# Kernel tuning notes

Measured on AMD Instinct MI355X. Metric: run time of the kernel, lower is better.

Reference implementation:

```python
import jax, jax.numpy as jnp
import numpy as np

D_IN = 1024
D_OUT = 1024
NUM_HEADS = 16
DIM_HEAD = D_OUT // NUM_HEADS


def setup_inputs() -> dict:
    key = jax.random.key(0)
    ks = jax.random.split(key, 6)
    s = 0.02
    x = jax.random.normal(ks[0], (2, 2048, D_IN), dtype=jnp.float32)
    Wk = jax.random.normal(ks[1], (D_IN, D_OUT), dtype=jnp.float32) * s
    Wq = jax.random.normal(ks[2], (D_IN, D_OUT), dtype=jnp.float32) * s
    Wv = jax.random.normal(ks[3], (D_IN, D_OUT), dtype=jnp.float32) * s
    Wo = jax.random.normal(ks[4], (D_OUT, D_OUT), dtype=jnp.float32) * s
    bo = jax.random.normal(ks[5], (D_OUT,), dtype=jnp.float32) * s
    return {"x": x, "Wk": Wk, "Wq": Wq, "Wv": Wv, "Wo": Wo, "bo": bo}


def reference(x, Wk, Wq, Wv, Wo, bo):
    B, S, _ = x.shape
    # projections -> [B, H, S, Dh]
    def split_heads(t):
        return t.reshape(B, S, NUM_HEADS, DIM_HEAD).transpose(0, 2, 1, 3)
    q = split_heads(x @ Wq)
    k = split_heads(x @ Wk)
    v = split_heads(x @ Wv)
    # NOTE: source uses non-in-place masked_fill whose result is discarded,
    # so NO causal mask is actually applied (faithful reproduction).
    scores = jnp.einsum("bhqd,bhkd->bhqk", q, k) / jnp.sqrt(jnp.float32(DIM_HEAD))
    wgts = jax.nn.softmax(scores, axis=-1)  # dropout = identity (eval mode)
    ctx = jnp.einsum("bhqk,bhkd->bhqd", wgts, v)
    ctx = ctx.transpose(0, 2, 1, 3).reshape(B, S, D_OUT)
    return ctx @ Wo + bo
```

## Files before the change

kernel.cpp:

```cpp
#include <hip/hip_runtime.h>
#include <stdint.h>

typedef short bf16x8 __attribute__((ext_vector_type(8)));
typedef float f32x4  __attribute__((ext_vector_type(4)));
typedef unsigned int u32x4 __attribute__((ext_vector_type(4)));
typedef unsigned int u32x2 __attribute__((ext_vector_type(2)));

__device__ __forceinline__ unsigned short f2bf(float f) {
  unsigned int u = __builtin_bit_cast(unsigned int, f) + 0x8000u;
  return (unsigned short)(u >> 16);
}
__device__ __forceinline__ unsigned int pack2bf(float a, float b) {
  unsigned int ua = __builtin_bit_cast(unsigned int, a) + 0x8000u;
  unsigned int ub = __builtin_bit_cast(unsigned int, b) + 0x8000u;
  return __builtin_amdgcn_perm(ub, ua, 0x07060302);
}

__device__ __forceinline__ void gl2lds16(const void* g, void* l) {
  __builtin_amdgcn_global_load_lds(
      (const __attribute__((address_space(1))) void*)g,
      (__attribute__((address_space(3))) void*)l, 16, 0, 0);
}

template <int N> __device__ __forceinline__ void wait_vmcnt() {
  asm volatile("s_waitcnt vmcnt(%0)" ::"n"(N) : "memory");
}

__global__ __launch_bounds__(256) void cast_x_k(const float* __restrict__ x,
                                                unsigned short* __restrict__ xb) {
  int i = blockIdx.x * 256 + threadIdx.x;
  float4 v = ((const float4*)x)[i];
  u32x2 o;
  o.x = pack2bf(v.x, v.y);
  o.y = pack2bf(v.z, v.w);
  ((u32x2*)xb)[i] = o;
}

__global__ __launch_bounds__(256) void castT_k(
    const float* __restrict__ Wq, const float* __restrict__ Wk,
    const float* __restrict__ Wv, const float* __restrict__ Wo,
    unsigned short* __restrict__ Tq, unsigned short* __restrict__ Tk,
    unsigned short* __restrict__ Tv, unsigned short* __restrict__ To) {
  __shared__ float tile[32][33];
  const int z = blockIdx.z;
  const float* W = (z == 0) ? Wq : (z == 1) ? Wk : (z == 2) ? Wv : Wo;
  unsigned short* T = (z == 0) ? Tq : (z == 1) ? Tk : (z == 2) ? Tv : To;
  const int tx = threadIdx.x, ty = threadIdx.y;
  const int n0 = blockIdx.x * 32, k0 = blockIdx.y * 32;
#pragma unroll
  for (int j = 0; j < 32; j += 8)
    tile[ty + j][tx] = W[(size_t)(k0 + ty + j) * 1024 + n0 + tx];
  __syncthreads();
#pragma unroll
  for (int j = 0; j < 32; j += 8)
    T[(size_t)(n0 + ty + j) * 1024 + k0 + tx] = f2bf(tile[tx][ty + j]);
}

template <int MODE, int TN>
__global__ __launch_bounds__(256, 2) void gemm_bt_k(const unsigned short* __restrict__ A,
                                                    const unsigned short* __restrict__ B,
                                                    void* __restrict__ C,
                                                    const float* __restrict__ bias,
                                                    int K) {
  __shared__ alignas(16) short lA[4][512 * 8];
  __shared__ alignas(16) short lB[4][128 * TN * 8];
  constexpr int PT = 2 + TN / 2;
  const int tid = threadIdx.x;
  const int wid = tid >> 6, lane = tid & 63;
  const int l15 = lane & 15, quad = lane >> 4;
  const int waveM = wid >> 1, waveN = wid & 1;
  const int bm = blockIdx.y * 128, bn = blockIdx.x * (32 * TN);

  f32x4 acc[4][TN];
#pragma unroll
  for (int i = 0; i < 4; ++i)
#pragma unroll
    for (int j = 0; j < TN; ++j) acc[i][j] = (f32x4){0.f, 0.f, 0.f, 0.f};

  auto stage = [&](int kk, short* la, short* lb) {
#pragma unroll
    for (int j = 0; j < 2; ++j) {
      int c = tid + 256 * j;
      int row = ((c >> 6) << 4) | (c & 15);
      int ch = (c >> 4) & 3;
      gl2lds16(A + (size_t)(bm + row) * K + kk + ch * 8, &la[(c & ~63) * 8]);
    }
#pragma unroll
    for (int j = 0; j < TN / 2; ++j) {
      int c = tid + 256 * j;
      int row = ((c >> 6) << 4) | (c & 15);
      int ch = (c >> 4) & 3;
      gl2lds16(B + (size_t)(bn + row) * K + kk + ch * 8, &lb[(c & ~63) * 8]);
    }
  };

  auto compute = [&](const short* la, const short* lb) {
    bf16x8 af[4], bfr[TN];
#pragma unroll
    for (int i = 0; i < 4; ++i)
      af[i] = *(const bf16x8*)&la[(((waveM * 4 + i) * 64) + lane) * 8];
#pragma unroll
    for (int j = 0; j < TN; ++j)
      bfr[j] = *(const bf16x8*)&lb[(((waveN * TN + j) * 64) + lane) * 8];
#pragma unroll
    for (int i = 0; i < 4; ++i)
#pragma unroll
      for (int j = 0; j < TN; ++j)
        acc[i][j] = __builtin_amdgcn_mfma_f32_16x16x32_bf16(af[i], bfr[j], acc[i][j], 0, 0, 0);
  };

  const int NT = K >> 5;
  short *pa0 = lA[0], *pa1 = lA[1], *pa2 = lA[2], *pa3 = lA[3];
  short *pb0 = lB[0], *pb1 = lB[1], *pb2 = lB[2], *pb3 = lB[3];
  stage(0, pa0, pb0);
  stage(32, pa1, pb1);
#pragma unroll 1
  for (int t = 0; t < NT - 2; ++t) {
    stage((t + 2) * 32, pa2, pb2);
    wait_vmcnt<2 * PT>();
    __builtin_amdgcn_sched_barrier(0);
    __builtin_amdgcn_s_barrier();
    __builtin_amdgcn_sched_barrier(0);
    compute(pa0, pb0);
    short* ta = pa0; pa0 = pa1; pa1 = pa2; pa2 = pa3; pa3 = ta;
    short* tb = pb0; pb0 = pb1; pb1 = pb2; pb2 = pb3; pb3 = tb;
  }
  wait_vmcnt<PT>();
  __builtin_amdgcn_sched_barrier(0);
  __builtin_amdgcn_s_barrier();
  __builtin_amdgcn_sched_barrier(0);
  compute(pa0, pb0);
  { short* ta = pa0; pa0 = pa1; pa1 = pa2; pa2 = pa3; pa3 = ta;
    short* tb = pb0; pb0 = pb1; pb1 = pb2; pb2 = pb3; pb3 = tb; }
  wait_vmcnt<0>();
  __builtin_amdgcn_sched_barrier(0);
  __builtin_amdgcn_s_barrier();
  __builtin_amdgcn_sched_barrier(0);
  compute(pa0, pb0);

#pragma unroll
  for (int i = 0; i < 4; ++i)
#pragma unroll
    for (int j = 0; j < TN; ++j) {
      int row = bm + waveM * 64 + i * 16 + quad * 4;
      int col = bn + (waveN * TN + j) * 16 + l15;
      if (MODE == 0) {
        unsigned short* Cq = (unsigned short*)C;
        int w = col >> 10, n1 = col & 1023;
        int h = n1 >> 6, d = n1 & 63;
        int b = row >> 11, s = row & 2047;
        int bhh = (b << 4) + h;
        if (w == 2) {
          int g = (i << 2) + quad;
          int ks2 = g >> 3, rem = g & 7;
          int pos = ((ks2 << 2) + (rem & 3)) * 8 + (rem >> 2) * 4;
          u32x2 pk;
          pk.x = pack2bf(acc[i][j][0], acc[i][j][1]);
          pk.y = pack2bf(acc[i][j][2], acc[i][j][3]);
          *(u32x2*)&Cq[(size_t)2 * 4194304 + ((size_t)bhh * 64 + d) * 2048 +
                       (s & ~63) + pos] = pk;
        } else {
          float sc = (w == 0) ? 0.18033688011112042f : 1.0f;
#pragma unroll
          for (int r = 0; r < 4; ++r)
            Cq[(size_t)w * 4194304 + ((size_t)bhh * 2048 + s + r) * 64 + d] =
                f2bf(acc[i][j][r] * sc);
        }
      } else {
#pragma unroll
        for (int r = 0; r < 4; ++r)
          ((float*)C)[(size_t)(row + r) * 1024 + col] = acc[i][j][r] + bias[col];
      }
    }
}

__global__ __launch_bounds__(256, 2) void flash_k(const unsigned short* __restrict__ Qh,
                                                  const unsigned short* __restrict__ Kh,
                                                  const unsigned short* __restrict__ Vt,
                                                  unsigned short* __restrict__ ctxb) {
  constexpr int SL = 2048;
  __shared__ alignas(16) short kt[4][512 * 8];
  __shared__ alignas(16) short vt[4][512 * 8];

  const int tid = threadIdx.x;
  const int wid = tid >> 6, lane = tid & 63;
  const int l15 = lane & 15, quad = lane >> 4;
  const int bid = blockIdx.x;
  const int jj = bid >> 3;
  const int bh = ((bid & 7) << 2) | (jj >> 4);
  const int q0 = (jj & 15) * 128 + wid * 32;

  const unsigned short* Qb = Qh + (size_t)bh * SL * 64;
  const unsigned short* Kb = Kh + (size_t)bh * SL * 64;
  const unsigned short* Vb = Vt + (size_t)bh * 64 * SL;

  bf16x8 qf[2][2];
#pragma unroll
  for (int s = 0; s < 2; ++s)
#pragma unroll
    for (int ks = 0; ks < 2; ++ks)
      qf[s][ks] = *(const bf16x8*)(Qb + (size_t)(q0 + s * 16 + l15) * 64 + ks * 32 + quad * 8);

  f32x4 o[2][4];
  f32x4 rs4[2] = {(f32x4){0.f, 0.f, 0.f, 0.f}, (f32x4){0.f, 0.f, 0.f, 0.f}};
  const f32x4 z4 = (f32x4){0.f, 0.f, 0.f, 0.f};
#pragma unroll
  for (int s = 0; s < 2; ++s)
#pragma unroll
    for (int t = 0; t < 4; ++t) o[s][t] = z4;

  auto stage = [&](int kb, short* ktb, short* vtb) {
#pragma unroll
    for (int j2 = 0; j2 < 2; ++j2) {
      int cc = tid + 256 * j2;
      int row = cc >> 3;
      int ko = (cc & 7) ^ (row & 7);
      gl2lds16(Kb + (size_t)(kb + row) * 64 + ko * 8, &ktb[(cc & ~63) * 8]);
      gl2lds16(Vb + (size_t)row * SL + kb + ko * 8, &vtb[(cc & ~63) * 8]);
    }
  };

  auto compute = [&](const short* ktb, const short* vtb) {
    f32x4 sv[2][4];
#pragma unroll
    for (int t = 0; t < 4; ++t) {
      int key = t * 16 + l15;
      bf16x8 kf0 = *(bf16x8*)&ktb[(key * 8 + (quad ^ (key & 7))) * 8];
      bf16x8 kf1 = *(bf16x8*)&ktb[(key * 8 + ((4 + quad) ^ (key & 7))) * 8];
#pragma unroll
      for (int s = 0; s < 2; ++s) {
        sv[s][t] = __builtin_amdgcn_mfma_f32_16x16x32_bf16(kf0, qf[s][0], z4, 0, 0, 0);
        sv[s][t] = __builtin_amdgcn_mfma_f32_16x16x32_bf16(kf1, qf[s][1], sv[s][t], 0, 0, 0);
      }
    }
    u32x4 pf[2][2];
#pragma unroll
    for (int s = 0; s < 2; ++s)
#pragma unroll
      for (int t = 0; t < 4; ++t) {
        f32x4 p;
#pragma unroll
        for (int r = 0; r < 4; ++r) p[r] = __builtin_amdgcn_exp2f(sv[s][t][r]);
        rs4[s] += p;
        pf[s][t >> 1][(t & 1) * 2 + 0] = pack2bf(p[0], p[1]);
        pf[s][t >> 1][(t & 1) * 2 + 1] = pack2bf(p[2], p[3]);
      }
#pragma unroll
    for (int t = 0; t < 4; ++t) {
      int d = t * 16 + l15;
#pragma unroll
      for (int ks = 0; ks < 2; ++ks) {
        bf16x8 vf = *(bf16x8*)&vtb[(d * 8 + ((ks * 4 + quad) ^ (d & 7))) * 8];
#pragma unroll
        for (int s = 0; s < 2; ++s)
          o[s][t] = __builtin_amdgcn_mfma_f32_16x16x32_bf16(
              vf, __builtin_bit_cast(bf16x8, pf[s][ks]), o[s][t], 0, 0, 0);
      }
    }
  };

  short *k0 = kt[0], *k1 = kt[1], *k2 = kt[2], *k3 = kt[3];
  short *v0 = vt[0], *v1 = vt[1], *v2 = vt[2], *v3 = vt[3];
  stage(0, k0, v0);
  stage(64, k1, v1);
#pragma unroll 1
  for (int t = 0; t < 30; ++t) {
    stage((t + 2) * 64, k2, v2);
    wait_vmcnt<8>();
    __builtin_amdgcn_sched_barrier(0);
    __builtin_amdgcn_s_barrier();
    __builtin_amdgcn_sched_barrier(0);
    compute(k0, v0);
    short* tk = k0; k0 = k1; k1 = k2; k2 = k3; k3 = tk;
    short* tv = v0; v0 = v1; v1 = v2; v2 = v3; v3 = tv;
  }
  wait_vmcnt<4>();
  __builtin_amdgcn_sched_barrier(0);
  __builtin_amdgcn_s_barrier();
  __builtin_amdgcn_sched_barrier(0);
  compute(k0, v0);
  { short* tk = k0; k0 = k1; k1 = k2; k2 = k3; k3 = tk;
    short* tv = v0; v0 = v1; v1 = v2; v2 = v3; v3 = tv; }
  wait_vmcnt<0>();
  __builtin_amdgcn_sched_barrier(0);
  __builtin_amdgcn_s_barrier();
  __builtin_amdgcn_sched_barrier(0);
  compute(k0, v0);

  const int bb = bh >> 4, h = bh & 15;
#pragma unroll
  for (int s = 0; s < 2; ++s) {
    float v = (rs4[s][0] + rs4[s][1]) + (rs4[s][2] + rs4[s][3]);
    v += __shfl_xor(v, 16);
    v += __shfl_xor(v, 32);
    float inv = 1.0f / v;
    int tok = q0 + s * 16 + l15;
    size_t base = ((size_t)(bb * 2048 + tok)) * 1024 + h * 64;
#pragma unroll
    for (int t = 0; t < 4; ++t) {
      u32x2 pk;
      pk.x = pack2bf(o[s][t][0] * inv, o[s][t][1] * inv);
      pk.y = pack2bf(o[s][t][2] * inv, o[s][t][3] * inv);
      *(u32x2*)&ctxb[base + t * 16 + quad * 4] = pk;
    }
  }
}

extern "C" void kernel_launch(void* const* d_in, const int* in_sizes, int n_in,
                              void* d_out, int out_size, void* d_ws, size_t ws_size,
                              hipStream_t stream) {
  const float* x  = (const float*)d_in[0];
  const float* Wk = (const float*)d_in[1];
  const float* Wq = (const float*)d_in[2];
  const float* Wv = (const float*)d_in[3];
  const float* Wo = (const float*)d_in[4];
  const float* bo = (const float*)d_in[5];
  float* out = (float*)d_out;

  char* ws = (char*)d_ws;
  const size_t MB = 1u << 20;
  unsigned short* xb   = (unsigned short*)(ws);
  unsigned short* WqT  = (unsigned short*)(ws + 8  * MB);
  unsigned short* WkT  = (unsigned short*)(ws + 10 * MB);
  unsigned short* WvT  = (unsigned short*)(ws + 12 * MB);
  unsigned short* WoT  = (unsigned short*)(ws + 14 * MB);
  unsigned short* Qh   = (unsigned short*)(ws + 16 * MB);
  unsigned short* ctxb = xb;

  cast_x_k<<<4096, 256, 0, stream>>>(x, xb);
  castT_k<<<dim3(32, 32, 4), dim3(32, 8), 0, stream>>>(Wq, Wk, Wv, Wo, WqT, WkT, WvT, WoT);
  gemm_bt_k<0, 6><<<dim3(16, 32), 256, 0, stream>>>(xb, WqT, Qh, nullptr, 1024);
  flash_k<<<512, 256, 0, stream>>>(Qh, Qh + 4194304, Qh + 2 * 4194304, ctxb);
  gemm_bt_k<1, 2><<<dim3(16, 32), 256, 0, stream>>>(ctxb, WoT, out, bo, 1024);
}
```

Before: 198.1 us.

## Enlarge GEMM N-tiles with configurable wave layout and add MFMA setprio

Generalizes the GEMM kernel over waves-per-N and thread count. The QKV projection now uses 512-thread blocks with a 384-wide N tile, and the output projection uses a 128-wide N tile instead of 64. Both halve the grid and raise A-tile reuse, which cuts global traffic for the activation matrix. It also wraps the MFMA sections in the GEMM and flash kernels with s_setprio so matrix work is favoured over other waves. The cost is fewer blocks in flight, higher register pressure, and vmcnt constants hardwired on the assumption that each thread issues 4 loads per stage.

Result: faster. 193.2 us (-2.5%).

```diff
diff --git a/kernel.cpp b/kernel.cpp
--- a/kernel.cpp
+++ b/kernel.cpp
@@ -56,20 +56,23 @@
     T[(size_t)(n0 + ty + j) * 1024 + k0 + tx] = f2bf(tile[tx][ty + j]);
 }
 
-template <int MODE, int TN>
-__global__ __launch_bounds__(256, 2) void gemm_bt_k(const unsigned short* __restrict__ A,
-                                                    const unsigned short* __restrict__ B,
-                                                    void* __restrict__ C,
-                                                    const float* __restrict__ bias,
-                                                    int K) {
+template <int MODE, int TN, int WN, int NTHR>
+__global__ __launch_bounds__(NTHR, 2) void gemm_bt_k(const unsigned short* __restrict__ A,
+                                                     const unsigned short* __restrict__ B,
+                                                     void* __restrict__ C,
+                                                     const float* __restrict__ bias,
+                                                     int K) {
+  constexpr int BN = WN * TN * 16;
+  constexpr int ALD = 512 / NTHR;
+  constexpr int BLD = BN * 4 / NTHR;
+  static_assert(ALD + BLD == 4, "PT must be 4 (vmcnt constants)");
   __shared__ alignas(16) short lA[4][512 * 8];
-  __shared__ alignas(16) short lB[4][128 * TN * 8];
-  constexpr int PT = 2 + TN / 2;
+  __shared__ alignas(16) short lB[4][BN * 4 * 8];
   const int tid = threadIdx.x;
   const int wid = tid >> 6, lane = tid & 63;
   const int l15 = lane & 15, quad = lane >> 4;
-  const int waveM = wid >> 1, waveN = wid & 1;
-  const int bm = blockIdx.y * 128, bn = blockIdx.x * (32 * TN);
+  const int waveM = wid / WN, waveN = wid % WN;
+  const int bm = blockIdx.y * 128, bn = blockIdx.x * BN;
 
   f32x4 acc[4][TN];
 #pragma unroll
@@ -79,15 +82,15 @@
 
   auto stage = [&](int kk, short* la, short* lb) {
 #pragma unroll
-    for (int j = 0; j < 2; ++j) {
-      int c = tid + 256 * j;
+    for (int j = 0; j < ALD; ++j) {
+      int c = tid + NTHR * j;
       int row = ((c >> 6) << 4) | (c & 15);
       int ch = (c >> 4) & 3;
       gl2lds16(A + (size_t)(bm + row) * K + kk + ch * 8, &la[(c & ~63) * 8]);
     }
 #pragma unroll
-    for (int j = 0; j < TN / 2; ++j) {
-      int c = tid + 256 * j;
+    for (int j = 0; j < BLD; ++j) {
+      int c = tid + NTHR * j;
       int row = ((c >> 6) << 4) | (c & 15);
       int ch = (c >> 4) & 3;
       gl2lds16(B + (size_t)(bn + row) * K + kk + ch * 8, &lb[(c & ~63) * 8]);
@@ -102,11 +105,13 @@
 #pragma unroll
     for (int j = 0; j < TN; ++j)
       bfr[j] = *(const bf16x8*)&lb[(((waveN * TN + j) * 64) + lane) * 8];
+    __builtin_amdgcn_s_setprio(1);
 #pragma unroll
     for (int i = 0; i < 4; ++i)
 #pragma unroll
       for (int j = 0; j < TN; ++j)
         acc[i][j] = __builtin_amdgcn_mfma_f32_16x16x32_bf16(af[i], bfr[j], acc[i][j], 0, 0, 0);
+    __builtin_amdgcn_s_setprio(0);
   };
 
   const int NT = K >> 5;
@@ -117,7 +122,7 @@
 #pragma unroll 1
   for (int t = 0; t < NT - 2; ++t) {
     stage((t + 2) * 32, pa2, pb2);
-    wait_vmcnt<2 * PT>();
+    wait_vmcnt<8>();
     __builtin_amdgcn_sched_barrier(0);
     __builtin_amdgcn_s_barrier();
     __builtin_amdgcn_sched_barrier(0);
@@ -125,7 +130,7 @@
     short* ta = pa0; pa0 = pa1; pa1 = pa2; pa2 = pa3; pa3 = ta;
     short* tb = pb0; pb0 = pb1; pb1 = pb2; pb2 = pb3; pb3 = tb;
   }
-  wait_vmcnt<PT>();
+  wait_vmcnt<4>();
   __builtin_amdgcn_sched_barrier(0);
   __builtin_amdgcn_s_barrier();
   __builtin_amdgcn_sched_barrier(0);
@@ -222,6 +227,7 @@
 
   auto compute = [&](const short* ktb, const short* vtb) {
     f32x4 sv[2][4];
+    __builtin_amdgcn_s_setprio(1);
 #pragma unroll
     for (int t = 0; t < 4; ++t) {
       int key = t * 16 + l15;
@@ -233,6 +239,7 @@
         sv[s][t] = __builtin_amdgcn_mfma_f32_16x16x32_bf16(kf1, qf[s][1], sv[s][t], 0, 0, 0);
       }
     }
+    __builtin_amdgcn_s_setprio(0);
     u32x4 pf[2][2];
 #pragma unroll
     for (int s = 0; s < 2; ++s)
@@ -245,6 +252,7 @@
         pf[s][t >> 1][(t & 1) * 2 + 0] = pack2bf(p[0], p[1]);
         pf[s][t >> 1][(t & 1) * 2 + 1] = pack2bf(p[2], p[3]);
       }
+    __builtin_amdgcn_s_setprio(1);
 #pragma unroll
     for (int t = 0; t < 4; ++t) {
       int d = t * 16 + l15;
@@ -257,6 +265,7 @@
               vf, __builtin_bit_cast(bf16x8, pf[s][ks]), o[s][t], 0, 0, 0);
       }
     }
+    __builtin_amdgcn_s_setprio(0);
   };
 
   short *k0 = kt[0], *k1 = kt[1], *k2 = kt[2], *k3 = kt[3];
@@ -329,7 +338,7 @@
 
   cast_x_k<<<4096, 256, 0, stream>>>(x, xb);
   castT_k<<<dim3(32, 32, 4), dim3(32, 8), 0, stream>>>(Wq, Wk, Wv, Wo, WqT, WkT, WvT, WoT);
-  gemm_bt_k<0, 6><<<dim3(16, 32), 256, 0, stream>>>(xb, WqT, Qh, nullptr, 1024);
+  gemm_bt_k<0, 6, 4, 512><<<dim3(8, 32), 512, 0, stream>>>(xb, WqT, Qh, nullptr, 1024);
   flash_k<<<512, 256, 0, stream>>>(Qh, Qh + 4194304, Qh + 2 * 4194304, ctxb);
-  gemm_bt_k<1, 2><<<dim3(16, 32), 256, 0, stream>>>(ctxb, WoT, out, bo, 1024);
-}
+  gemm_bt_k<1, 4, 2, 256><<<dim3(8, 32), 256, 0, stream>>>(ctxb, WoT, out, bo, 1024);
+}
```
